# Performance work log

Measured on AMD Instinct MI355X. Metric: run time of the kernel, lower is better.

Reference implementation:

```python
import jax, jax.numpy as jnp
import numpy as np

N = 8192
D_IN = 512
D_HID = 256
D_OUT = 128
NEG_SLOPE = 0.25
MASK_VAL = -1.0e12
EDGE_PROB = 0.004  # avg degree ~33


def _leaky(x):
    return jax.nn.leaky_relu(x, NEG_SLOPE)


def setup_inputs() -> dict:
    key = jax.random.key(0)
    ks = jax.random.split(key, 9)
    x = jax.random.normal(ks[0], (N, D_IN), jnp.float32)
    # sparse-ish normalized adjacency, stored dense (torch uses sparse mm / to_dense)
    vals = jax.random.uniform(ks[1], (N, N), jnp.float32)
    mask = jax.random.uniform(ks[2], (N, N)) < EDGE_PROB
    adj = jnp.where(mask, vals, 0.0).astype(jnp.float32)
    W1 = jax.random.normal(ks[3], (D_IN, D_HID), jnp.float32) * (2.0 / (D_IN + D_HID)) ** 0.5
    b1 = jnp.zeros((D_HID,), jnp.float32)
    W2 = jax.random.normal(ks[4], (D_HID, D_HID), jnp.float32) * (1.0 / D_HID) ** 0.5
    b2 = jnp.zeros((D_HID,), jnp.float32)
    Wg = jax.random.normal(ks[5], (D_HID, D_OUT), jnp.float32) * (2.0 / (D_HID + D_OUT)) ** 0.5
    a = jax.random.normal(ks[6], (2 * D_OUT, 1), jnp.float32) * 0.1
    return dict(x=x, adj=adj, W1=W1, b1=b1, W2=W2, b2=b2, Wg=Wg, a=a)


def reference(x, adj, W1, b1, W2, b2, Wg, a):
    # GCN layer 1: adj @ (x @ W1) + b1, leaky_relu (dropout p=0 / eval -> identity)
    x1 = _leaky(adj @ (x @ W1) + b1)
    # GCN layer 2
    x2 = _leaky(adj @ (x1 @ W2) + b2)
    # GAT layer: h = x2 @ Wg; e[i,j] = leaky_relu([h_i || h_j] @ a)
    # identical to leaky_relu((h@a1)_i + (h@a2)_j) without the O(N^2*2F) concat
    h = x2 @ Wg                              # [N, D_OUT]
    a1 = a[:D_OUT, 0]
    a2 = a[D_OUT:, 0]
    e = _leaky((h @ a1)[:, None] + (h @ a2)[None, :])  # [N, N]
    att = jnp.where(adj > 0, e, MASK_VAL)
    att = jax.nn.softmax(att, axis=1)
    h_prime = att @ h                        # [N, D_OUT] (concat=False -> no elu)
    out = _leaky(h_prime)
    mu = out[:, : D_OUT // 2]
    logvar = out[:, D_OUT // 2 :]
    return mu, logvar
```

## Files before the change

kernel.cpp:

```cpp
#include <hip/hip_runtime.h>

typedef unsigned short u16;
typedef u16 u16x4 __attribute__((ext_vector_type(4)));
typedef __bf16 bf16x8 __attribute__((ext_vector_type(8)));
typedef float f32x4 __attribute__((ext_vector_type(4)));

#define NROW 8192
#define CAP 128
#define D_IN 512
#define D_HID 256
#define D_OUT 128

__device__ __forceinline__ float leaky_f(float x) { return x > 0.f ? x : 0.25f * x; }

__device__ __forceinline__ u16 f2bf_rne(float f) {
  unsigned u = __float_as_uint(f);
  u += 0x7fffu + ((u >> 16) & 1u);
  return (u16)(u >> 16);
}
__device__ __forceinline__ float bf2f(u16 v) { return __uint_as_float(((unsigned)v) << 16); }
__device__ __forceinline__ void split_bf16(float f, u16& hi, u16& lo) {
  hi = f2bf_rne(f);
  float fh = __uint_as_float(((unsigned)hi) << 16);
  lo = f2bf_rne(f - fh);
}

__global__ __launch_bounds__(256) void k_packw(
    const float* __restrict__ W1, u16* __restrict__ B1,
    const float* __restrict__ W2, u16* __restrict__ B2,
    const float* __restrict__ Wg, u16* __restrict__ B3) {
  const float* W; u16* Bt; int K, Nc, idx;
  int pb = blockIdx.x;
  if (pb < 64)      { W = W1; Bt = B1; K = D_IN;  Nc = D_HID; idx = pb * 256 + threadIdx.x; }
  else if (pb < 96) { W = W2; Bt = B2; K = D_HID; Nc = D_HID; idx = (pb - 64) * 256 + threadIdx.x; }
  else              { W = Wg; Bt = B3; K = D_HID; Nc = D_OUT; idx = (pb - 96) * 256 + threadIdx.x; }
  int ko8 = K >> 3;
  int n = idx / ko8, k0 = (idx % ko8) << 3;
  alignas(16) u16 hh[8], ll[8];
#pragma unroll
  for (int j = 0; j < 8; ++j) {
    float f = W[(size_t)(k0 + j) * Nc + n];
    split_bf16(f, hh[j], ll[j]);
  }
  size_t ro = (size_t)n * 2 * K;
  *(uint4*)(Bt + ro + k0)     = *(const uint4*)hh;
  *(uint4*)(Bt + ro + K + k0) = *(const uint4*)ll;
}

__global__ __launch_bounds__(256) void k_csr_gemm1(const float* __restrict__ adj,
    int* __restrict__ cnt, int* __restrict__ cols, float* __restrict__ vals,
    const float* __restrict__ X, const u16* __restrict__ Bt, float* __restrict__ C) {
  __shared__ u16 Ah[64 * 40], Al[64 * 40];
  __shared__ u16 Bh[64 * 40], Bl[64 * 40];
  __shared__ int csrc;
  int b = blockIdx.x;
  int tid = threadIdx.x;
  if (b < 512) {
    const int N = D_HID, K = D_IN;
    int bm = (b >> 2) * 64, bn = (b & 3) * 64;
    int wave = tid >> 6, lane = tid & 63, l15 = lane & 15, quad = lane >> 4;
    f32x4 acc[4] = {};
    int ar = tid >> 2, aj = (tid & 3) << 3;
    const float* Xrow = X + (size_t)(bm + ar) * K + aj;
    const u16* Brow = Bt + (size_t)(bn + ar) * (2 * K) + aj;
    for (int k0 = 0; k0 < K; k0 += 32) {
      alignas(16) u16 hh[8], ll[8];
      float xv[8];
      *(float4*)(xv)     = *(const float4*)(Xrow + k0);
      *(float4*)(xv + 4) = *(const float4*)(Xrow + k0 + 4);
#pragma unroll
      for (int e = 0; e < 8; ++e) split_bf16(xv[e], hh[e], ll[e]);
      *(uint4*)(&Ah[ar * 40 + aj]) = *(const uint4*)hh;
      *(uint4*)(&Al[ar * 40 + aj]) = *(const uint4*)ll;
      *(uint4*)(&Bh[ar * 40 + aj]) = *(const uint4*)(Brow + k0);
      *(uint4*)(&Bl[ar * 40 + aj]) = *(const uint4*)(Brow + K + k0);
      __syncthreads();
      bf16x8 afh = *(const bf16x8*)(&Ah[(wave * 16 + l15) * 40 + quad * 8]);
      bf16x8 afl = *(const bf16x8*)(&Al[(wave * 16 + l15) * 40 + quad * 8]);
#pragma unroll
      for (int c = 0; c < 4; ++c) {
        bf16x8 bfh = *(const bf16x8*)(&Bh[(c * 16 + l15) * 40 + quad * 8]);
        bf16x8 bfl = *(const bf16x8*)(&Bl[(c * 16 + l15) * 40 + quad * 8]);
        acc[c] = __builtin_amdgcn_mfma_f32_16x16x32_bf16(afh, bfh, acc[c], 0, 0, 0);
        acc[c] = __builtin_amdgcn_mfma_f32_16x16x32_bf16(afh, bfl, acc[c], 0, 0, 0);
        acc[c] = __builtin_amdgcn_mfma_f32_16x16x32_bf16(afl, bfh, acc[c], 0, 0, 0);
      }
      __syncthreads();
    }
#pragma unroll
    for (int c = 0; c < 4; ++c)
#pragma unroll
      for (int rg = 0; rg < 4; ++rg) {
        int rowi = bm + wave * 16 + quad * 4 + rg;
        int coli = bn + c * 16 + l15;
        C[(size_t)rowi * N + coli] = acc[c][rg];
      }
    return;
  }
  int i = b - 512;
  if (tid == 0) csrc = 0;
  __syncthreads();
  const float4* row = (const float4*)(adj + (size_t)i * NROW);
  for (int j4 = tid; j4 < NROW / 4; j4 += 256) {
    float4 v = row[j4];
    int base = j4 * 4;
    if (v.x > 0.f) { int s = atomicAdd(&csrc, 1); if (s < CAP) { cols[i*CAP+s] = base;   vals[i*CAP+s] = v.x; } }
    if (v.y > 0.f) { int s = atomicAdd(&csrc, 1); if (s < CAP) { cols[i*CAP+s] = base+1; vals[i*CAP+s] = v.y; } }
    if (v.z > 0.f) { int s = atomicAdd(&csrc, 1); if (s < CAP) { cols[i*CAP+s] = base+2; vals[i*CAP+s] = v.z; } }
    if (v.w > 0.f) { int s = atomicAdd(&csrc, 1); if (s < CAP) { cols[i*CAP+s] = base+3; vals[i*CAP+s] = v.w; } }
  }
  __syncthreads();
  if (tid == 0) cnt[i] = (csrc < CAP) ? csrc : CAP;
}

__global__ __launch_bounds__(256) void k_gemm(const u16* __restrict__ A, const u16* __restrict__ Bt,
    float* __restrict__ C, int N, int K) {
  __shared__ u16 Ah[64 * 40], Al[64 * 40];
  __shared__ u16 Bh[64 * 40], Bl[64 * 40];
  int tid = threadIdx.x;
  int bm = blockIdx.y * 64, bn = blockIdx.x * 64;
  int wave = tid >> 6, lane = tid & 63, l15 = lane & 15, quad = lane >> 4;
  f32x4 acc[4] = {};
  int ar = tid >> 2, aj = (tid & 3) << 3;
  const u16* Arow = A + (size_t)(bm + ar) * (2 * K) + aj;
  const u16* Brow = Bt + (size_t)(bn + ar) * (2 * K) + aj;
  for (int k0 = 0; k0 < K; k0 += 32) {
    *(uint4*)(&Ah[ar * 40 + aj]) = *(const uint4*)(Arow + k0);
    *(uint4*)(&Al[ar * 40 + aj]) = *(const uint4*)(Arow + K + k0);
    *(uint4*)(&Bh[ar * 40 + aj]) = *(const uint4*)(Brow + k0);
    *(uint4*)(&Bl[ar * 40 + aj]) = *(const uint4*)(Brow + K + k0);
    __syncthreads();
    bf16x8 afh = *(const bf16x8*)(&Ah[(wave * 16 + l15) * 40 + quad * 8]);
    bf16x8 afl = *(const bf16x8*)(&Al[(wave * 16 + l15) * 40 + quad * 8]);
#pragma unroll
    for (int c = 0; c < 4; ++c) {
      bf16x8 bfh = *(const bf16x8*)(&Bh[(c * 16 + l15) * 40 + quad * 8]);
      bf16x8 bfl = *(const bf16x8*)(&Bl[(c * 16 + l15) * 40 + quad * 8]);
      acc[c] = __builtin_amdgcn_mfma_f32_16x16x32_bf16(afh, bfh, acc[c], 0, 0, 0);
      acc[c] = __builtin_amdgcn_mfma_f32_16x16x32_bf16(afh, bfl, acc[c], 0, 0, 0);
      acc[c] = __builtin_amdgcn_mfma_f32_16x16x32_bf16(afl, bfh, acc[c], 0, 0, 0);
    }
    __syncthreads();
  }
#pragma unroll
  for (int c = 0; c < 4; ++c)
#pragma unroll
    for (int rg = 0; rg < 4; ++rg) {
      int rowi = bm + wave * 16 + quad * 4 + rg;
      int coli = bn + c * 16 + l15;
      C[(size_t)rowi * N + coli] = acc[c][rg];
    }
}

__global__ __launch_bounds__(256) void k_gemm3(const u16* __restrict__ A, const u16* __restrict__ Bt,
    u16* __restrict__ Hb, int K,
    const float* __restrict__ aptr, float* __restrict__ s1, float* __restrict__ s2) {
  __shared__ u16 Ah[32 * 40], Al[32 * 40];
  __shared__ u16 Bh[128 * 40], Bl[128 * 40];
  __shared__ float sp1[2][32], sp2[2][32];
  int tid = threadIdx.x;
  int bm = blockIdx.y * 32;
  int wave = tid >> 6, lane = tid & 63, l15 = lane & 15, quad = lane >> 4;
  int rhalf = wave >> 1, chalf = wave & 1;
  f32x4 acc[4] = {};
  int t7 = tid & 127;
  int ar = t7 >> 2, aj = (t7 & 3) << 3;
  int br = tid >> 1, bj = (tid & 1) << 4;
  const u16* Arow = A + (size_t)(bm + ar) * (2 * K) + aj + (tid < 128 ? 0 : K);
  u16* Adst = (tid < 128 ? Ah : Al) + ar * 40 + aj;
  const u16* Brow = Bt + (size_t)br * (2 * K) + bj;
  for (int k0 = 0; k0 < K; k0 += 32) {
    *(uint4*)Adst = *(const uint4*)(Arow + k0);
#pragma unroll
    for (int jj = 0; jj < 2; ++jj) {
      *(uint4*)(&Bh[br * 40 + bj + jj * 8]) = *(const uint4*)(Brow + k0 + jj * 8);
      *(uint4*)(&Bl[br * 40 + bj + jj * 8]) = *(const uint4*)(Brow + K + k0 + jj * 8);
    }
    __syncthreads();
    bf16x8 afh = *(const bf16x8*)(&Ah[(rhalf * 16 + l15) * 40 + quad * 8]);
    bf16x8 afl = *(const bf16x8*)(&Al[(rhalf * 16 + l15) * 40 + quad * 8]);
#pragma unroll
    for (int c = 0; c < 4; ++c) {
      bf16x8 bfh = *(const bf16x8*)(&Bh[(chalf * 64 + c * 16 + l15) * 40 + quad * 8]);
      bf16x8 bfl = *(const bf16x8*)(&Bl[(chalf * 64 + c * 16 + l15) * 40 + quad * 8]);
      acc[c] = __builtin_amdgcn_mfma_f32_16x16x32_bf16(afh, bfh, acc[c], 0, 0, 0);
      acc[c] = __builtin_amdgcn_mfma_f32_16x16x32_bf16(afh, bfl, acc[c], 0, 0, 0);
      acc[c] = __builtin_amdgcn_mfma_f32_16x16x32_bf16(afl, bfh, acc[c], 0, 0, 0);
    }
    __syncthreads();
  }
#pragma unroll
  for (int c = 0; c < 4; ++c)
#pragma unroll
    for (int rg = 0; rg < 4; ++rg) {
      int rowi = bm + rhalf * 16 + quad * 4 + rg;
      int coli = chalf * 64 + c * 16 + l15;
      Hb[(size_t)rowi * 128 + coli] = f2bf_rne(acc[c][rg]);
    }
  float a1v[4], a2v[4];
#pragma unroll
  for (int c = 0; c < 4; ++c) {
    a1v[c] = aptr[chalf * 64 + c * 16 + l15];
    a2v[c] = aptr[128 + chalf * 64 + c * 16 + l15];
  }
#pragma unroll
  for (int rg = 0; rg < 4; ++rg) {
    float p1 = 0.f, p2 = 0.f;
#pragma unroll
    for (int c = 0; c < 4; ++c) { p1 = fmaf(acc[c][rg], a1v[c], p1); p2 = fmaf(acc[c][rg], a2v[c], p2); }
#pragma unroll
    for (int m = 1; m < 16; m <<= 1) { p1 += __shfl_xor(p1, m); p2 += __shfl_xor(p2, m); }
    if (l15 == 0) {
      int rloc = rhalf * 16 + quad * 4 + rg;
      sp1[chalf][rloc] = p1; sp2[chalf][rloc] = p2;
    }
  }
  __syncthreads();
  if (tid < 32) {
    s1[bm + tid] = sp1[0][tid] + sp1[1][tid];
    s2[bm + tid] = sp2[0][tid] + sp2[1][tid];
  }
}

__global__ __launch_bounds__(256) void k_spmm_pack(const float* __restrict__ Hin,
    const float* __restrict__ bias, const int* __restrict__ cnt,
    const int* __restrict__ cols, const float* __restrict__ vals, u16* __restrict__ Ap) {
  __shared__ int sc[4][CAP];
  __shared__ float sv[4][CAP];
  int w = threadIdx.x >> 6, lane = threadIdx.x & 63;
  int i = blockIdx.x * 4 + w;
  int n = cnt[i];
  if (lane < n)      { sc[w][lane]      = cols[i * CAP + lane];      sv[w][lane]      = vals[i * CAP + lane]; }
  if (lane + 64 < n) { sc[w][lane + 64] = cols[i * CAP + lane + 64]; sv[w][lane + 64] = vals[i * CAP + lane + 64]; }
  __syncthreads();
  const float4* H4 = (const float4*)Hin;
  float4 acc = {0.f, 0.f, 0.f, 0.f};
  int k = 0;
  for (; k + 7 < n; k += 8) {
    int   c0 = sc[w][k],     c1 = sc[w][k + 1], c2 = sc[w][k + 2], c3 = sc[w][k + 3];
    int   c4 = sc[w][k + 4], c5 = sc[w][k + 5], c6 = sc[w][k + 6], c7 = sc[w][k + 7];
    float w0 = sv[w][k],     w1 = sv[w][k + 1], w2 = sv[w][k + 2], w3 = sv[w][k + 3];
    float w4 = sv[w][k + 4], w5 = sv[w][k + 5], w6 = sv[w][k + 6], w7 = sv[w][k + 7];
    float4 v0 = H4[(size_t)c0 * 64 + lane];
    float4 v1 = H4[(size_t)c1 * 64 + lane];
    float4 v2 = H4[(size_t)c2 * 64 + lane];
    float4 v3 = H4[(size_t)c3 * 64 + lane];
    float4 v4 = H4[(size_t)c4 * 64 + lane];
    float4 v5 = H4[(size_t)c5 * 64 + lane];
    float4 v6 = H4[(size_t)c6 * 64 + lane];
    float4 v7 = H4[(size_t)c7 * 64 + lane];
    acc.x = fmaf(w0, v0.x, acc.x); acc.y = fmaf(w0, v0.y, acc.y); acc.z = fmaf(w0, v0.z, acc.z); acc.w = fmaf(w0, v0.w, acc.w);
    acc.x = fmaf(w1, v1.x, acc.x); acc.y = fmaf(w1, v1.y, acc.y); acc.z = fmaf(w1, v1.z, acc.z); acc.w = fmaf(w1, v1.w, acc.w);
    acc.x = fmaf(w2, v2.x, acc.x); acc.y = fmaf(w2, v2.y, acc.y); acc.z = fmaf(w2, v2.z, acc.z); acc.w = fmaf(w2, v2.w, acc.w);
    acc.x = fmaf(w3, v3.x, acc.x); acc.y = fmaf(w3, v3.y, acc.y); acc.z = fmaf(w3, v3.z, acc.z); acc.w = fmaf(w3, v3.w, acc.w);
    acc.x = fmaf(w4, v4.x, acc.x); acc.y = fmaf(w4, v4.y, acc.y); acc.z = fmaf(w4, v4.z, acc.z); acc.w = fmaf(w4, v4.w, acc.w);
    acc.x = fmaf(w5, v5.x, acc.x); acc.y = fmaf(w5, v5.y, acc.y); acc.z = fmaf(w5, v5.z, acc.z); acc.w = fmaf(w5, v5.w, acc.w);
    acc.x = fmaf(w6, v6.x, acc.x); acc.y = fmaf(w6, v6.y, acc.y); acc.z = fmaf(w6, v6.z, acc.z); acc.w = fmaf(w6, v6.w, acc.w);
    acc.x = fmaf(w7, v7.x, acc.x); acc.y = fmaf(w7, v7.y, acc.y); acc.z = fmaf(w7, v7.z, acc.z); acc.w = fmaf(w7, v7.w, acc.w);
  }
  for (; k < n; ++k) {
    float wv = sv[w][k];
    float4 v = H4[(size_t)sc[w][k] * 64 + lane];
    acc.x = fmaf(wv, v.x, acc.x); acc.y = fmaf(wv, v.y, acc.y);
    acc.z = fmaf(wv, v.z, acc.z); acc.w = fmaf(wv, v.w, acc.w);
  }
  float4 bv = ((const float4*)bias)[lane];
  float r[4] = { leaky_f(acc.x + bv.x), leaky_f(acc.y + bv.y),
                 leaky_f(acc.z + bv.z), leaky_f(acc.w + bv.w) };
  u16x4 hi4, lo4;
#pragma unroll
  for (int e = 0; e < 4; ++e) { u16 hh, ll; split_bf16(r[e], hh, ll); hi4[e] = hh; lo4[e] = ll; }
  size_t ro = (size_t)i * 512;
  *(u16x4*)(Ap + ro + 4 * lane) = hi4;
  *(u16x4*)(Ap + ro + 256 + 4 * lane) = lo4;
}

__global__ __launch_bounds__(256) void k_attn(const u16* __restrict__ Hb,
    const float* __restrict__ s1, const float* __restrict__ s2,
    const int* __restrict__ cnt, const int* __restrict__ cols, float* __restrict__ out) {
  __shared__ int sc[4][CAP];
  __shared__ float sp[4][CAP];
  int w = threadIdx.x >> 6, lane = threadIdx.x & 63;
  int i = blockIdx.x * 4 + w;
  int n = cnt[i];
  float s1i = s1[i];
  float e0 = -1e30f, e1 = -1e30f;
  if (lane < n)      { int c = cols[i * CAP + lane];      sc[w][lane]      = c; e0 = leaky_f(s1i + s2[c]); }
  if (lane + 64 < n) { int c = cols[i * CAP + lane + 64]; sc[w][lane + 64] = c; e1 = leaky_f(s1i + s2[c]); }
  float m = fmaxf(e0, e1);
#pragma unroll
  for (int o = 32; o > 0; o >>= 1) m = fmaxf(m, __shfl_xor(m, o));
  float p0 = (lane < n)      ? expf(e0 - m) : 0.f;
  float p1 = (lane + 64 < n) ? expf(e1 - m) : 0.f;
  if (lane < n)      sp[w][lane]      = p0;
  if (lane + 64 < n) sp[w][lane + 64] = p1;
  float s = p0 + p1;
#pragma unroll
  for (int o = 32; o > 0; o >>= 1) s += __shfl_xor(s, o);
  float inv = (n > 0) ? 1.0f / s : 0.f;
  __syncthreads();
  int half = lane >> 5, t32 = lane & 31;
  float4 acc = {0.f, 0.f, 0.f, 0.f};
  int k = half;
  for (; k + 6 < n; k += 8) {
    int   c0 = sc[w][k],     c1 = sc[w][k + 2], c2 = sc[w][k + 4], c3 = sc[w][k + 6];
    float w0 = sp[w][k],     w1 = sp[w][k + 2], w2 = sp[w][k + 4], w3 = sp[w][k + 6];
    u16x4 a0 = *(const u16x4*)(Hb + (size_t)c0 * 128 + 4 * t32);
    u16x4 a1 = *(const u16x4*)(Hb + (size_t)c1 * 128 + 4 * t32);
    u16x4 a2 = *(const u16x4*)(Hb + (size_t)c2 * 128 + 4 * t32);
    u16x4 a3 = *(const u16x4*)(Hb + (size_t)c3 * 128 + 4 * t32);
    acc.x = fmaf(w0, bf2f(a0[0]), acc.x); acc.y = fmaf(w0, bf2f(a0[1]), acc.y);
    acc.z = fmaf(w0, bf2f(a0[2]), acc.z); acc.w = fmaf(w0, bf2f(a0[3]), acc.w);
    acc.x = fmaf(w1, bf2f(a1[0]), acc.x); acc.y = fmaf(w1, bf2f(a1[1]), acc.y);
    acc.z = fmaf(w1, bf2f(a1[2]), acc.z); acc.w = fmaf(w1, bf2f(a1[3]), acc.w);
    acc.x = fmaf(w2, bf2f(a2[0]), acc.x); acc.y = fmaf(w2, bf2f(a2[1]), acc.y);
    acc.z = fmaf(w2, bf2f(a2[2]), acc.z); acc.w = fmaf(w2, bf2f(a2[3]), acc.w);
    acc.x = fmaf(w3, bf2f(a3[0]), acc.x); acc.y = fmaf(w3, bf2f(a3[1]), acc.y);
    acc.z = fmaf(w3, bf2f(a3[2]), acc.z); acc.w = fmaf(w3, bf2f(a3[3]), acc.w);
  }
  for (; k < n; k += 2) {
    float wv = sp[w][k];
    u16x4 a = *(const u16x4*)(Hb + (size_t)sc[w][k] * 128 + 4 * t32);
    acc.x = fmaf(wv, bf2f(a[0]), acc.x); acc.y = fmaf(wv, bf2f(a[1]), acc.y);
    acc.z = fmaf(wv, bf2f(a[2]), acc.z); acc.w = fmaf(wv, bf2f(a[3]), acc.w);
  }
  acc.x += __shfl_xor(acc.x, 32);
  acc.y += __shfl_xor(acc.y, 32);
  acc.z += __shfl_xor(acc.z, 32);
  acc.w += __shfl_xor(acc.w, 32);
  if (lane < 32) {
    float4 r;
    r.x = leaky_f(acc.x * inv);
    r.y = leaky_f(acc.y * inv);
    r.z = leaky_f(acc.z * inv);
    r.w = leaky_f(acc.w * inv);
    float4* o4 = (float4*)out;
    if (lane < 16) o4[(size_t)i * 16 + lane] = r;
    else           o4[(size_t)NROW * 16 + (size_t)i * 16 + (lane - 16)] = r;
  }
}

extern "C" void kernel_launch(void* const* d_in, const int* in_sizes, int n_in,
                              void* d_out, int out_size, void* d_ws, size_t ws_size,
                              hipStream_t stream) {
  const float* x   = (const float*)d_in[0];
  const float* adj = (const float*)d_in[1];
  const float* W1  = (const float*)d_in[2];
  const float* b1  = (const float*)d_in[3];
  const float* W2  = (const float*)d_in[4];
  const float* b2  = (const float*)d_in[5];
  const float* Wg  = (const float*)d_in[6];
  const float* a   = (const float*)d_in[7];
  float* out = (float*)d_out;

  char* ws = (char*)d_ws;
  int*   row_cnt  = (int*)  (ws + 0);
  int*   row_cols = (int*)  (ws + 32768);
  float* row_vals = (float*)(ws + 4227072);
  u16*   B1t      = (u16*)  (ws + 8421376);
  u16*   B2t      = (u16*)  (ws + 8945664);
  u16*   B3t      = (u16*)  (ws + 9207808);
  float* s1       = (float*)(ws + 9338880);
  float* s2       = (float*)(ws + 9371648);
  u16*   hbf      = (u16*)  (ws + 9404416);
  float* H0T2     = (float*)(ws + 13598720);
  u16*   Apack    = (u16*)  (ws + 21987328);

  k_packw<<<112, 256, 0, stream>>>(W1, B1t, W2, B2t, Wg, B3t);
  k_csr_gemm1<<<512 + NROW, 256, 0, stream>>>(adj, row_cnt, row_cols, row_vals, x, B1t, H0T2);
  k_spmm_pack<<<NROW / 4, 256, 0, stream>>>(H0T2, b1, row_cnt, row_cols, row_vals, Apack);
  k_gemm<<<dim3(4, 128), 256, 0, stream>>>(Apack, B2t, H0T2, D_HID, D_HID);
  k_spmm_pack<<<NROW / 4, 256, 0, stream>>>(H0T2, b2, row_cnt, row_cols, row_vals, Apack);
  k_gemm3<<<dim3(1, 256), 256, 0, stream>>>(Apack, B3t, hbf, D_HID, a, s1, s2);
  k_attn<<<NROW / 4, 256, 0, stream>>>(hbf, s1, s2, row_cnt, row_cols, out);
}
```

Before: 463.5 us.

## Store dense GEMM outputs as bf16 and use wave-ballot CSR compaction

The intermediate X@W1 and X1@W2 results are now written as bf16 instead of fp32, and the SpMM gather kernel reads bf16 rows and converts them to float. This halves the bytes of the random row gathers in the two sparse aggregations and the bytes of the GEMM writes. The CSR build replaces per-element shared atomics with one wave-level ballot, popcount and a single atomic per wave. The cost is lost precision in the intermediate features, which previously went through a split hi/lo path, and the order of the column lists changes.

```diff
diff --git a/kernel.cpp b/kernel.cpp
--- a/kernel.cpp
+++ b/kernel.cpp
@@ -49,7 +49,7 @@
 
 __global__ __launch_bounds__(256) void k_csr_gemm1(const float* __restrict__ adj,
     int* __restrict__ cnt, int* __restrict__ cols, float* __restrict__ vals,
-    const float* __restrict__ X, const u16* __restrict__ Bt, float* __restrict__ C) {
+    const float* __restrict__ X, const u16* __restrict__ Bt, u16* __restrict__ C) {
   __shared__ u16 Ah[64 * 40], Al[64 * 40];
   __shared__ u16 Bh[64 * 40], Bl[64 * 40];
   __shared__ int csrc;
@@ -93,28 +93,44 @@
       for (int rg = 0; rg < 4; ++rg) {
         int rowi = bm + wave * 16 + quad * 4 + rg;
         int coli = bn + c * 16 + l15;
-        C[(size_t)rowi * N + coli] = acc[c][rg];
+        C[(size_t)rowi * N + coli] = f2bf_rne(acc[c][rg]);
       }
     return;
   }
   int i = b - 512;
   if (tid == 0) csrc = 0;
   __syncthreads();
+  int lane = tid & 63;
   const float4* row = (const float4*)(adj + (size_t)i * NROW);
   for (int j4 = tid; j4 < NROW / 4; j4 += 256) {
     float4 v = row[j4];
     int base = j4 * 4;
-    if (v.x > 0.f) { int s = atomicAdd(&csrc, 1); if (s < CAP) { cols[i*CAP+s] = base;   vals[i*CAP+s] = v.x; } }
-    if (v.y > 0.f) { int s = atomicAdd(&csrc, 1); if (s < CAP) { cols[i*CAP+s] = base+1; vals[i*CAP+s] = v.y; } }
-    if (v.z > 0.f) { int s = atomicAdd(&csrc, 1); if (s < CAP) { cols[i*CAP+s] = base+2; vals[i*CAP+s] = v.z; } }
-    if (v.w > 0.f) { int s = atomicAdd(&csrc, 1); if (s < CAP) { cols[i*CAP+s] = base+3; vals[i*CAP+s] = v.w; } }
+    bool p0 = v.x > 0.f, p1 = v.y > 0.f, p2 = v.z > 0.f, p3 = v.w > 0.f;
+    unsigned long long m0 = __ballot(p0), m1 = __ballot(p1);
+    unsigned long long m2 = __ballot(p2), m3 = __ballot(p3);
+    int c0 = __popcll(m0), c1 = __popcll(m1), c2 = __popcll(m2), c3 = __popcll(m3);
+    int tot = c0 + c1 + c2 + c3;
+    if (tot) {
+      int wbase = 0;
+      if (lane == 0) wbase = atomicAdd(&csrc, tot);
+      wbase = __shfl(wbase, 0);
+      unsigned long long lm = (1ULL << lane) - 1ULL;
+      int o0 = wbase + __popcll(m0 & lm);
+      int o1 = wbase + c0 + __popcll(m1 & lm);
+      int o2 = wbase + c0 + c1 + __popcll(m2 & lm);
+      int o3 = wbase + c0 + c1 + c2 + __popcll(m3 & lm);
+      if (p0 && o0 < CAP) { cols[i*CAP+o0] = base;   vals[i*CAP+o0] = v.x; }
+      if (p1 && o1 < CAP) { cols[i*CAP+o1] = base+1; vals[i*CAP+o1] = v.y; }
+      if (p2 && o2 < CAP) { cols[i*CAP+o2] = base+2; vals[i*CAP+o2] = v.z; }
+      if (p3 && o3 < CAP) { cols[i*CAP+o3] = base+3; vals[i*CAP+o3] = v.w; }
+    }
   }
   __syncthreads();
   if (tid == 0) cnt[i] = (csrc < CAP) ? csrc : CAP;
 }
 
 __global__ __launch_bounds__(256) void k_gemm(const u16* __restrict__ A, const u16* __restrict__ Bt,
-    float* __restrict__ C, int N, int K) {
+    u16* __restrict__ C, int N, int K) {
   __shared__ u16 Ah[64 * 40], Al[64 * 40];
   __shared__ u16 Bh[64 * 40], Bl[64 * 40];
   int tid = threadIdx.x;
@@ -148,7 +164,7 @@
     for (int rg = 0; rg < 4; ++rg) {
       int rowi = bm + wave * 16 + quad * 4 + rg;
       int coli = bn + c * 16 + l15;
-      C[(size_t)rowi * N + coli] = acc[c][rg];
+      C[(size_t)rowi * N + coli] = f2bf_rne(acc[c][rg]);
     }
 }
 
@@ -222,7 +238,7 @@
   }
 }
 
-__global__ __launch_bounds__(256) void k_spmm_pack(const float* __restrict__ Hin,
+__global__ __launch_bounds__(256) void k_spmm_pack(const u16* __restrict__ Hin,
     const float* __restrict__ bias, const int* __restrict__ cnt,
     const int* __restrict__ cols, const float* __restrict__ vals, u16* __restrict__ Ap) {
   __shared__ int sc[4][CAP];
@@ -233,7 +249,6 @@
   if (lane < n)      { sc[w][lane]      = cols[i * CAP + lane];      sv[w][lane]      = vals[i * CAP + lane]; }
   if (lane + 64 < n) { sc[w][lane + 64] = cols[i * CAP + lane + 64]; sv[w][lane + 64] = vals[i * CAP + lane + 64]; }
   __syncthreads();
-  const float4* H4 = (const float4*)Hin;
   float4 acc = {0.f, 0.f, 0.f, 0.f};
   int k = 0;
   for (; k + 7 < n; k += 8) {
@@ -241,28 +256,36 @@
     int   c4 = sc[w][k + 4], c5 = sc[w][k + 5], c6 = sc[w][k + 6], c7 = sc[w][k + 7];
     float w0 = sv[w][k],     w1 = sv[w][k + 1], w2 = sv[w][k + 2], w3 = sv[w][k + 3];
     float w4 = sv[w][k + 4], w5 = sv[w][k + 5], w6 = sv[w][k + 6], w7 = sv[w][k + 7];
-    float4 v0 = H4[(size_t)c0 * 64 + lane];
-    float4 v1 = H4[(size_t)c1 * 64 + lane];
-    float4 v2 = H4[(size_t)c2 * 64 + lane];
-    float4 v3 = H4[(size_t)c3 * 64 + lane];
-    float4 v4 = H4[(size_t)c4 * 64 + lane];
-    float4 v5 = H4[(size_t)c5 * 64 + lane];
-    float4 v6 = H4[(size_t)c6 * 64 + lane];
-    float4 v7 = H4[(size_t)c7 * 64 + lane];
-    acc.x = fmaf(w0, v0.x, acc.x); acc.y = fmaf(w0, v0.y, acc.y); acc.z = fmaf(w0, v0.z, acc.z); acc.w = fmaf(w0, v0.w, acc.w);
-    acc.x = fmaf(w1, v1.x, acc.x); acc.y = fmaf(w1, v1.y, acc.y); acc.z = fmaf(w1, v1.z, acc.z); acc.w = fmaf(w1, v1.w, acc.w);
-    acc.x = fmaf(w2, v2.x, acc.x); acc.y = fmaf(w2, v2.y, acc.y); acc.z = fmaf(w2, v2.z, acc.z); acc.w = fmaf(w2, v2.w, acc.w);
-    acc.x = fmaf(w3, v3.x, acc.x); acc.y = fmaf(w3, v3.y, acc.y); acc.z = fmaf(w3, v3.z, acc.z); acc.w = fmaf(w3, v3.w, acc.w);
-    acc.x = fmaf(w4, v4.x, acc.x); acc.y = fmaf(w4, v4.y, acc.y); acc.z = fmaf(w4, v4.z, acc.z); acc.w = fmaf(w4, v4.w, acc.w);
-    acc.x = fmaf(w5, v5.x, acc.x); acc.y = fmaf(w5, v5.y, acc.y); acc.z = fmaf(w5, v5.z, acc.z); acc.w = fmaf(w5, v5.w, acc.w);
-    acc.x = fmaf(w6, v6.x, acc.x); acc.y = fmaf(w6, v6.y, acc.y); acc.z = fmaf(w6, v6.z, acc.z); acc.w = fmaf(w6, v6.w, acc.w);
-    acc.x = fmaf(w7, v7.x, acc.x); acc.y = fmaf(w7, v7.y, acc.y); acc.z = fmaf(w7, v7.z, acc.z); acc.w = fmaf(w7, v7.w, acc.w);
+    u16x4 v0 = *(const u16x4*)(Hin + (size_t)c0 * 256 + 4 * lane);
+    u16x4 v1 = *(const u16x4*)(Hin + (size_t)c1 * 256 + 4 * lane);
+    u16x4 v2 = *(const u16x4*)(Hin + (size_t)c2 * 256 + 4 * lane);
+    u16x4 v3 = *(const u16x4*)(Hin + (size_t)c3 * 256 + 4 * lane);
+    u16x4 v4 = *(const u16x4*)(Hin + (size_t)c4 * 256 + 4 * lane);
+    u16x4 v5 = *(const u16x4*)(Hin + (size_t)c5 * 256 + 4 * lane);
+    u16x4 v6 = *(const u16x4*)(Hin + (size_t)c6 * 256 + 4 * lane);
+    u16x4 v7 = *(const u16x4*)(Hin + (size_t)c7 * 256 + 4 * lane);
+    acc.x = fmaf(w0, bf2f(v0[0]), acc.x); acc.y = fmaf(w0, bf2f(v0[1]), acc.y);
+    acc.z = fmaf(w0, bf2f(v0[2]), acc.z); acc.w = fmaf(w0, bf2f(v0[3]), acc.w);
+    acc.x = fmaf(w1, bf2f(v1[0]), acc.x); acc.y = fmaf(w1, bf2f(v1[1]), acc.y);
+    acc.z = fmaf(w1, bf2f(v1[2]), acc.z); acc.w = fmaf(w1, bf2f(v1[3]), acc.w);
+    acc.x = fmaf(w2, bf2f(v2[0]), acc.x); acc.y = fmaf(w2, bf2f(v2[1]), acc.y);
+    acc.z = fmaf(w2, bf2f(v2[2]), acc.z); acc.w = fmaf(w2, bf2f(v2[3]), acc.w);
+    acc.x = fmaf(w3, bf2f(v3[0]), acc.x); acc.y = fmaf(w3, bf2f(v3[1]), acc.y);
+    acc.z = fmaf(w3, bf2f(v3[2]), acc.z); acc.w = fmaf(w3, bf2f(v3[3]), acc.w);
+    acc.x = fmaf(w4, bf2f(v4[0]), acc.x); acc.y = fmaf(w4, bf2f(v4[1]), acc.y);
+    acc.z = fmaf(w4, bf2f(v4[2]), acc.z); acc.w = fmaf(w4, bf2f(v4[3]), acc.w);
+    acc.x = fmaf(w5, bf2f(v5[0]), acc.x); acc.y = fmaf(w5, bf2f(v5[1]), acc.y);
+    acc.z = fmaf(w5, bf2f(v5[2]), acc.z); acc.w = fmaf(w5, bf2f(v5[3]), acc.w);
+    acc.x = fmaf(w6, bf2f(v6[0]), acc.x); acc.y = fmaf(w6, bf2f(v6[1]), acc.y);
+    acc.z = fmaf(w6, bf2f(v6[2]), acc.z); acc.w = fmaf(w6, bf2f(v6[3]), acc.w);
+    acc.x = fmaf(w7, bf2f(v7[0]), acc.x); acc.y = fmaf(w7, bf2f(v7[1]), acc.y);
+    acc.z = fmaf(w7, bf2f(v7[2]), acc.z); acc.w = fmaf(w7, bf2f(v7[3]), acc.w);
   }
   for (; k < n; ++k) {
     float wv = sv[w][k];
-    float4 v = H4[(size_t)sc[w][k] * 64 + lane];
-    acc.x = fmaf(wv, v.x, acc.x); acc.y = fmaf(wv, v.y, acc.y);
-    acc.z = fmaf(wv, v.z, acc.z); acc.w = fmaf(wv, v.w, acc.w);
+    u16x4 v = *(const u16x4*)(Hin + (size_t)sc[w][k] * 256 + 4 * lane);
+    acc.x = fmaf(wv, bf2f(v[0]), acc.x); acc.y = fmaf(wv, bf2f(v[1]), acc.y);
+    acc.z = fmaf(wv, bf2f(v[2]), acc.z); acc.w = fmaf(wv, bf2f(v[3]), acc.w);
   }
   float4 bv = ((const float4*)bias)[lane];
   float r[4] = { leaky_f(acc.x + bv.x), leaky_f(acc.y + bv.y),
@@ -363,7 +386,7 @@
   float* s1       = (float*)(ws + 9338880);
   float* s2       = (float*)(ws + 9371648);
   u16*   hbf      = (u16*)  (ws + 9404416);
-  float* H0T2     = (float*)(ws + 13598720);
+  u16*   H0T2     = (u16*)  (ws + 13598720);
   u16*   Apack    = (u16*)  (ws + 21987328);
 
   k_packw<<<112, 256, 0, stream>>>(W1, B1t, W2, B2t, Wg, B3t);
```

Measured after the change: 442.7 us. -4.5%, faster.
